# Performance work log

Hardware: AMD Instinct MI355X
Metric: run time of the kernel (lower is better)

The kernel has to match this reference:

```python
import jax, jax.numpy as jnp
import numpy as np
from jax import lax

DN = ('NCDHW', 'OIDHW', 'NCDHW')
BN_EPS = 1e-5  # eval-mode BatchNorm3d with running_mean=0, running_var=1


def conv3d(x, w, b):
    y = lax.conv_general_dilated(x, w, window_strides=(1, 1, 1),
                                 padding=[(1, 1)] * 3, dimension_numbers=DN)
    return y + b[None, :, None, None, None]


def maxpool2(x):
    return lax.reduce_window(x, -jnp.inf, lax.max,
                             (1, 1, 2, 2, 2), (1, 1, 2, 2, 2), 'VALID')


def spline_block(x, cw, cb, knots, sw, w1, w2, g, beta):
    # SplineConv3d: conv -> (BSpline3D blend with SiLU) -> BN(eval) -> maxpool
    y = conv3d(x, cw, cb)                                   # [b,c,d,h,w]
    basis = jnp.maximum(y[..., None] - knots, 0.0) ** 3     # [b,c,d,h,w,k]
    sp = jnp.einsum('bcdhwk,ck->bcdhw', basis, sw)
    out = (w1[None, :, None, None, None] * sp
           + w2[None, :, None, None, None] * (y * jax.nn.sigmoid(y)))
    scale = (g / jnp.sqrt(1.0 + BN_EPS))[None, :, None, None, None]
    return maxpool2(out * scale + beta[None, :, None, None, None])


def setup_inputs() -> dict:
    key = jax.random.key(0)
    ks = iter(jax.random.split(key, 40))
    def nrm(shape, s=1.0):
        return jax.random.normal(next(ks), shape, dtype=jnp.float32) * s
    d = {}
    d['x'] = nrm((2, 1, 64, 64, 64))
    for cin, cout, t in [(1, 32, '1'), (32, 64, '2'), (64, 128, '3')]:
        d[f'c{t}_w'] = nrm((cout, cin, 3, 3, 3), 0.1)
        d[f'c{t}_b'] = nrm((cout,), 0.01)
        d[f'c{t}_knots'] = jnp.linspace(-1.0, 1.0, 10).astype(jnp.float32)
        d[f'c{t}_sw'] = nrm((cout, 10), 0.2)
        d[f'c{t}_w1'] = nrm((cout,), 0.2)
        d[f'c{t}_w2'] = nrm((cout,), 0.2)
        d[f'bn{t}_g'] = 1.0 + nrm((cout,), 0.1)
        d[f'bn{t}_b'] = nrm((cout,), 0.1)
    d['fc1_w'] = nrm((256, 128), 0.05)
    d['fc1_b'] = nrm((256,), 0.01)
    d['fc2_w'] = nrm((2, 256), 0.05)
    d['fc2_b'] = nrm((2,), 0.01)
    return d


def reference(x,
              c1_w, c1_b, c1_knots, c1_sw, c1_w1, c1_w2, bn1_g, bn1_b,
              c2_w, c2_b, c2_knots, c2_sw, c2_w1, c2_w2, bn2_g, bn2_b,
              c3_w, c3_b, c3_knots, c3_sw, c3_w1, c3_w2, bn3_g, bn3_b,
              fc1_w, fc1_b, fc2_w, fc2_b):
    h = spline_block(x, c1_w, c1_b, c1_knots, c1_sw, c1_w1, c1_w2, bn1_g, bn1_b)
    h = spline_block(h, c2_w, c2_b, c2_knots, c2_sw, c2_w1, c2_w2, bn2_g, bn2_b)
    h = spline_block(h, c3_w, c3_b, c3_knots, c3_sw, c3_w1, c3_w2, bn3_g, bn3_b)
    h = h.mean(axis=(2, 3, 4))          # AdaptiveAvgPool3d((1,1,1)) + flatten
    h = jax.nn.relu(h @ fc1_w.T + fc1_b)  # dropout is identity in eval mode
    return h @ fc2_w.T + fc2_b
```

## Files before the change

kernel.cpp:

```cpp
#include <hip/hip_runtime.h>
#include <math.h>


#define GLOBAL_AS __attribute__((address_space(1)))
#define LDS_AS    __attribute__((address_space(3)))

static __device__ __forceinline__ void async_ld16(const float* g, float* l) {
    __builtin_amdgcn_global_load_lds((const GLOBAL_AS void*)g, (LDS_AS void*)l,
                                     16, 0, 0);
}

__global__ __launch_bounds__(256) void repack_kernel(
    const float* __restrict__ w1, const float* __restrict__ w2,
    const float* __restrict__ w3,
    float* __restrict__ o1, float* __restrict__ o2, float* __restrict__ o3)
{
    const int i = blockIdx.x * 256 + threadIdx.x;
    const float* src;
    float* dst;
    if (i < 32)            { src = w1 + i * 27;           dst = o1 + i * 28; }
    else if (i < 2080)     { const int j = i - 32;   src = w2 + j * 27; dst = o2 + j * 28; }
    else if (i < 10272)    { const int j = i - 2080; src = w3 + j * 27; dst = o3 + j * 28; }
    else return;
#pragma unroll
    for (int t = 0; t < 27; t++) dst[t] = src[t];
    dst[27] = 0.0f;
}

template <int TPB_, int CIN, int CSPLIT, int G,
          int WDT, int WHT, int WWT, int BD, int BH, int BW>
__global__ __launch_bounds__(TPB_, 2) void spline_block_kernel(
    const float* __restrict__ x,
    const float4* __restrict__ wpk,
    const float* __restrict__ cb,
    const float* __restrict__ knots,
    const float* __restrict__ sw,
    const float* __restrict__ w1,
    const float* __restrict__ w2,
    const float* __restrict__ g,
    const float* __restrict__ beta,
    const float* __restrict__ zbuf,
    float* __restrict__ out,
    int N, int Cout, int D, int H, int W,
    int ntiles, int nthw, int ntw)
{
    constexpr int NSW    = BD * BH * BW;
    constexpr int NW     = TPB_ / 64;
    constexpr int CPG    = CIN / CSPLIT;
    constexpr int ID     = 2 * WDT + 2;
    constexpr int IH     = 2 * WHT + 2;
    constexpr int CHK    = (WWT + 4) / 2;
    constexpr int PITCH  = CHK * 4;
    constexpr int ROWS   = ID * IH;
    constexpr int CHUNKS = ROWS * CHK;
    constexpr int PHYS   = CHUNKS * 4;
    constexpr int NCH    = (CHUNKS + 63) / 64;
    constexpr int BUFS   = (CPG > 1) ? 2 : 1;
    static_assert(NW == NSW * CSPLIT, "waves = spatial-tiles x cin-split");
    static_assert(WDT * WHT * WWT == 64, "one wave per spatial tile");
    static_assert(CIN % CSPLIT == 0, "cin divisible");
    static_assert(G == 4, "weight half-loop assumes G==4");
    static_assert(NCH <= 32, "mask fits u32");
    static_assert(NCH == 6, "s_waitcnt vmcnt(6) literal assumes 6 issues/cin");
    static_assert(CSPLIT == 1 ||
                  (CSPLIT - 1) * 64 * G * 8 <= NW * BUFS * PHYS,
                  "reduction scratch fits in tile");

    __shared__ __align__(16) float tile[NW][BUFS][PHYS];
    __shared__ float4 stbl[G * 11];

    const int PD = D >> 1, PH = H >> 1, PW = W >> 1;
    const int groups = Cout / G;
    const int tid  = threadIdx.x;
    const int wv   = tid >> 6;
    const int lane = tid & 63;
    const int sw_  = wv % NSW;
    const int cg   = wv / NSW;

    const int bx      = blockIdx.x;
    const int tile_id = bx % ntiles;
    const int t1      = bx / ntiles;
    const int grp     = t1 % groups;
    const int n       = t1 / groups;
    const int c0      = grp * G;
    const int cinbase = cg * CPG;
    const int cinbase_u = __builtin_amdgcn_readfirstlane(cinbase);

    const int td  = tile_id / nthw;
    const int rem = tile_id % nthw;
    const int th_ = rem / ntw;
    const int tw_ = rem % ntw;

    for (int i = tid; i < G * 11; i += TPB_) {
        const int gg  = i / 11;
        const int cnt = i % 11;
        const int c   = c0 + gg;
        float A = 0.f, B3 = 0.f, C3 = 0.f, Dd = 0.f;
        for (int j = 0; j < cnt; j++) {
            const float s = sw[c * 10 + j];
            const float k = knots[j];
            A  += s;
            B3 += 3.0f * s * k;
            C3 += 3.0f * s * k * k;
            Dd += s * k * k * k;
        }
        stbl[i] = make_float4(A, B3, C3, Dd);
    }

    const int swd = sw_ / (BH * BW);
    const int r2  = sw_ % (BH * BW);
    const int swh = r2 / BW;
    const int sww = r2 % BW;
    const int pd0 = td  * (BD * WDT) + swd * WDT;
    const int ph0 = th_ * (BH * WHT) + swh * WHT;
    const int pw0 = tw_ * (BW * WWT) + sww * WWT;

    const int pwl = lane % WWT;
    const int phl = (lane / WWT) % WHT;
    const int pdl = lane / (WWT * WHT);

    const int d0 = 2 * pd0 - 1, h0 = 2 * ph0 - 1;
    const int w0 = 2 * pw0 - 1;
    const int wb = w0 & ~3;
    const int woff = w0 - wb;

    int off[NCH];
    unsigned vm = 0;
#pragma unroll
    for (int k = 0; k < NCH; k++) {
        const int chunk = lane + 64 * k;
        const int row = chunk / CHK, cs = chunk - row * CHK;
        const int dz = row / IH, hy = row - dz * IH;
        const int dd = d0 + dz, hh = h0 + hy;
        const int wsd = wb + cs * 4;
        const bool ok = (chunk < CHUNKS) &
                        ((unsigned)dd < (unsigned)D) &
                        ((unsigned)hh < (unsigned)H) &
                        ((unsigned)wsd < (unsigned)W);
        off[k] = ok ? (dd * H + hh) * W + wsd : 0;
        vm |= (unsigned)ok << k;
    }

    const size_t chstride = (size_t)D * H * W;
    const float* xn = x + (size_t)n * CIN * chstride;

    float acc[G][8];
#pragma unroll
    for (int gg = 0; gg < G; gg++)
#pragma unroll
        for (int i = 0; i < 8; i++) acc[gg][i] = 0.0f;

    __syncthreads();

    auto stage = [&](int ci, int buf) {
        const float* xc = xn + (size_t)ci * chstride;
        float* dst = &tile[wv][buf][0];
#pragma unroll
        for (int k = 0; k < NCH; k++) {
            const int chunk = lane + 64 * k;
            if ((k + 1) * 64 <= CHUNKS || chunk < CHUNKS) {
                const float* src = ((vm >> k) & 1) ? (xc + off[k]) : zbuf;
                async_ld16(src, dst + chunk * 4);
            }
        }
    };

    stage(cinbase_u, 0);

#pragma unroll 1
    for (int s = 0; s < CPG; s++) {
        const int cur = s & (BUFS - 1);
        if (s + 1 < CPG) {
            stage(cinbase_u + s + 1, cur ^ 1);
            asm volatile("s_waitcnt vmcnt(6)" ::: "memory");
        } else {
            asm volatile("s_waitcnt vmcnt(0)" ::: "memory");
        }

        const int ci_u = cinbase_u + s;
        const float4* wq = wpk + (size_t)(c0 * CIN + ci_u) * 7;

        const float* tb = &tile[wv][cur][0];
        float r[64];
#pragma unroll
        for (int dz = 0; dz < 4; dz++)
#pragma unroll
        for (int dy = 0; dy < 4; dy++) {
            const int rb = ((2 * pdl + dz) * IH + (2 * phl + dy)) * PITCH +
                           woff + 2 * pwl;
            r[(dz * 4 + dy) * 4 + 0] = tb[rb + 0];
            r[(dz * 4 + dy) * 4 + 1] = tb[rb + 1];
            r[(dz * 4 + dy) * 4 + 2] = tb[rb + 2];
            r[(dz * 4 + dy) * 4 + 3] = tb[rb + 3];
        }

#pragma unroll
        for (int half = 0; half < 2; half++) {
            float4 q[2][7];
#pragma unroll
            for (int gh = 0; gh < 2; gh++)
#pragma unroll
                for (int ch = 0; ch < 7; ch++)
                    q[gh][ch] = wq[(size_t)(half * 2 + gh) * (CIN * 7) + ch];
#pragma unroll
            for (int gh = 0; gh < 2; gh++) {
                const int gg = half * 2 + gh;
#pragma unroll
                for (int ch = 0; ch < 7; ch++) {
#pragma unroll
                    for (int j = 0; j < 4; j++) {
                        const int tap = ch * 4 + j;
                        if (tap < 27) {
                            const float wvj = (j == 0) ? q[gh][ch].x
                                            : (j == 1) ? q[gh][ch].y
                                            : (j == 2) ? q[gh][ch].z
                                            : q[gh][ch].w;
                            const int kd = tap / 9, kh = (tap % 9) / 3, kw = tap % 3;
#pragma unroll
                            for (int od = 0; od < 2; od++)
#pragma unroll
                            for (int oh = 0; oh < 2; oh++)
#pragma unroll
                            for (int ow = 0; ow < 2; ow++)
                                acc[gg][(od * 2 + oh) * 2 + ow] =
                                    fmaf(wvj,
                                         r[((od + kd) * 4 + (oh + kh)) * 4 + (ow + kw)],
                                         acc[gg][(od * 2 + oh) * 2 + ow]);
                        }
                    }
                }
            }
        }
    }

    float* af = &acc[0][0];
    if (CSPLIT > 1) {
        __syncthreads();
        float* scratch = &tile[0][0][0];
        if (cg > 0) {
#pragma unroll
            for (int idx = 0; idx < G * 8; idx++)
                scratch[(idx * (CSPLIT - 1) + (cg - 1)) * 64 + lane] = af[idx];
        }
        __syncthreads();
        if (cg == 0) {
#pragma unroll
            for (int idx = 0; idx < G * 8; idx++) {
                float s2 = af[idx];
                for (int j = 0; j < CSPLIT - 1; j++)
                    s2 += scratch[(idx * (CSPLIT - 1) + j) * 64 + lane];
                af[idx] = s2;
            }
        }
    }

    if (cg == 0) {
        const int pdg = pd0 + pdl, phg = ph0 + phl, pwg = pw0 + pwl;
#pragma unroll
        for (int gg = 0; gg < G; gg++) {
            const int c = c0 + gg;
            const float bias = cb[c];
            const float W1 = w1[c], W2 = w2[c];
            const float scale = g[c] * rsqrtf(1.0f + 1e-5f);
            const float bb = beta[c];

            float m = -INFINITY;
#pragma unroll
            for (int i = 0; i < 8; i++) {
                const float y = acc[gg][i] + bias;
                int idx = (int)floorf((y + 1.0f) * 4.5f) + 1;
                idx = min(max(idx, 0), 10);
                const float4 cf = stbl[gg * 11 + idx];
                const float sp = ((cf.x * y - cf.y) * y + cf.z) * y - cf.w;
                const float silu = y / (1.0f + __expf(-y));
                const float o = fmaf(W1 * sp + W2 * silu, scale, bb);
                m = fmaxf(m, o);
            }
            out[((size_t)(n * Cout + c) * PD + pdg) * PH * PW + phg * PW + pwg] = m;
        }
    }
}

__global__ __launch_bounds__(256) void head_kernel(
    const float* __restrict__ h,
    const float* __restrict__ fw1, const float* __restrict__ fb1,
    const float* __restrict__ fw2, const float* __restrict__ fb2,
    float* __restrict__ out)
{
    __shared__ float pooled[256];
    __shared__ float hbuf[2][256];
    const int tid = threadIdx.x, w = tid >> 6, lane = tid & 63;
    for (int p = w; p < 256; p += 4) {
        const float* row = h + (size_t)p * 512;
        float s = 0.0f;
#pragma unroll
        for (int i = 0; i < 8; i++) s += row[lane + 64 * i];
#pragma unroll
        for (int o = 32; o > 0; o >>= 1) s += __shfl_down(s, o, 64);
        if (lane == 0) pooled[p] = s * (1.0f / 512.0f);
    }
    __syncthreads();
    const int j = tid;
#pragma unroll
    for (int nn = 0; nn < 2; nn++) {
        float s = fb1[j];
        for (int k = 0; k < 128; k++)
            s = fmaf(pooled[nn * 128 + k], fw1[j * 128 + k], s);
        hbuf[nn][j] = fmaxf(s, 0.0f);
    }
    __syncthreads();
    const int wid = j >> 6, l2 = j & 63;
    const int nn = wid >> 1, oo = wid & 1;
    float s = 0.0f;
    for (int k = l2; k < 256; k += 64) s += hbuf[nn][k] * fw2[oo * 256 + k];
#pragma unroll
    for (int o = 32; o > 0; o >>= 1) s += __shfl_down(s, o, 64);
    if (l2 == 0) out[nn * 2 + oo] = s + fb2[oo];
}

extern "C" void kernel_launch(void* const* d_in, const int* in_sizes, int n_in,
                              void* d_out, int out_size, void* d_ws, size_t ws_size,
                              hipStream_t stream) {
    const float* x      = (const float*)d_in[0];
    const float* c1_w   = (const float*)d_in[1];
    const float* c1_b   = (const float*)d_in[2];
    const float* c1_kn  = (const float*)d_in[3];
    const float* c1_sw  = (const float*)d_in[4];
    const float* c1_w1  = (const float*)d_in[5];
    const float* c1_w2  = (const float*)d_in[6];
    const float* bn1_g  = (const float*)d_in[7];
    const float* bn1_b  = (const float*)d_in[8];
    const float* c2_w   = (const float*)d_in[9];
    const float* c2_b   = (const float*)d_in[10];
    const float* c2_kn  = (const float*)d_in[11];
    const float* c2_sw  = (const float*)d_in[12];
    const float* c2_w1  = (const float*)d_in[13];
    const float* c2_w2  = (const float*)d_in[14];
    const float* bn2_g  = (const float*)d_in[15];
    const float* bn2_b  = (const float*)d_in[16];
    const float* c3_w   = (const float*)d_in[17];
    const float* c3_b   = (const float*)d_in[18];
    const float* c3_kn  = (const float*)d_in[19];
    const float* c3_sw  = (const float*)d_in[20];
    const float* c3_w1  = (const float*)d_in[21];
    const float* c3_w2  = (const float*)d_in[22];
    const float* bn3_g  = (const float*)d_in[23];
    const float* bn3_b  = (const float*)d_in[24];
    const float* fc1_w  = (const float*)d_in[25];
    const float* fc1_b  = (const float*)d_in[26];
    const float* fc2_w  = (const float*)d_in[27];
    const float* fc2_b  = (const float*)d_in[28];

    float* ws = (float*)d_ws;
    float* h1     = ws;
    float* h2     = h1 + 2097152;
    float* h3     = h2 + 524288;
    float* pooled = h3 + 131072;
    float* zbuf   = pooled + 256;
    float* wp1    = zbuf + 16;
    float* wp2    = wp1 + 896;
    float* wp3    = wp2 + 57344;

    hipMemsetAsync(zbuf, 0, 64, stream);

    repack_kernel<<<dim3(41), dim3(256), 0, stream>>>(c1_w, c2_w, c3_w,
                                                      wp1, wp2, wp3);

    spline_block_kernel<128, 1, 1, 4, 2, 4, 8, 1, 1, 2>
        <<<dim3(4096), dim3(128), 0, stream>>>(
        x, (const float4*)wp1, c1_b, c1_kn, c1_sw, c1_w1, c1_w2, bn1_g, bn1_b,
        zbuf, h1, 2, 32, 64, 64, 64, 256, 16, 2);
    spline_block_kernel<128, 32, 2, 4, 2, 4, 8, 1, 1, 1>
        <<<dim3(2048), dim3(128), 0, stream>>>(
        h1, (const float4*)wp2, c2_b, c2_kn, c2_sw, c2_w1, c2_w2, bn2_g, bn2_b,
        zbuf, h2, 2, 64, 32, 32, 32, 64, 8, 2);
    spline_block_kernel<256, 64, 4, 4, 2, 4, 8, 1, 1, 1>
        <<<dim3(512), dim3(256), 0, stream>>>(
        h2, (const float4*)wp3, c3_b, c3_kn, c3_sw, c3_w1, c3_w2, bn3_g, bn3_b,
        zbuf, h3, 2, 128, 16, 16, 16, 8, 2, 1);
    head_kernel<<<dim3(1), dim3(256), 0, stream>>>(h3, fc1_w, fc1_b, fc2_w, fc2_b,
                                                   (float*)d_out);
}
```

Before: 369.5 us.

## Use zero-padded activation buffers to drop bounds masking and misaligned staging

```diff
diff --git a/kernel.cpp b/kernel.cpp
--- a/kernel.cpp
+++ b/kernel.cpp
@@ -10,21 +10,38 @@
                                      16, 0, 0);
 }
 
-__global__ __launch_bounds__(256) void repack_kernel(
+__global__ __launch_bounds__(256) void prep_kernel(
+    const float* __restrict__ x,
     const float* __restrict__ w1, const float* __restrict__ w2,
     const float* __restrict__ w3,
+    float* __restrict__ xp,
     float* __restrict__ o1, float* __restrict__ o2, float* __restrict__ o3)
 {
-    const int i = blockIdx.x * 256 + threadIdx.x;
-    const float* src;
-    float* dst;
-    if (i < 32)            { src = w1 + i * 27;           dst = o1 + i * 28; }
-    else if (i < 2080)     { const int j = i - 32;   src = w2 + j * 27; dst = o2 + j * 28; }
-    else if (i < 10272)    { const int j = i - 2080; src = w3 + j * 27; dst = o3 + j * 28; }
-    else return;
-#pragma unroll
-    for (int t = 0; t < 27; t++) dst[t] = src[t];
-    dst[27] = 0.0f;
+    const int b = blockIdx.x;
+    if (b < 41) {
+        const int i = b * 256 + threadIdx.x;
+        const float* src;
+        float* dst;
+        if (i < 32)         { src = w1 + i * 27;              dst = o1 + i * 28; }
+        else if (i < 2080)  { const int j = i - 32;    src = w2 + j * 27; dst = o2 + j * 28; }
+        else if (i < 10272) { const int j = i - 2080;  src = w3 + j * 27; dst = o3 + j * 28; }
+        else return;
+#pragma unroll
+        for (int t = 0; t < 27; t++) dst[t] = src[t];
+        dst[27] = 0.0f;
+    } else {
+        const int idx = (b - 41) * 256 + threadIdx.x;
+        if (idx >= 2 * 66 * 66 * 68) return;
+        const int wp = idx % 68;
+        int t = idx / 68;
+        const int hp = t % 66; t /= 66;
+        const int dp = t % 66;
+        const int nn = t / 66;
+        float v = 0.0f;
+        if (dp >= 1 && dp <= 64 && hp >= 1 && hp <= 64 && wp >= 1 && wp <= 64)
+            v = x[(((size_t)nn * 64 + dp - 1) * 64 + hp - 1) * 64 + wp - 1];
+        xp[idx] = v;
+    }
 }
 
 template <int TPB_, int CIN, int CSPLIT, int G,
@@ -39,9 +56,10 @@
     const float* __restrict__ w2,
     const float* __restrict__ g,
     const float* __restrict__ beta,
-    const float* __restrict__ zbuf,
     float* __restrict__ out,
-    int N, int Cout, int D, int H, int W,
+    int N, int Cout,
+    int ICH, int IHP, int IWP,
+    int ODP, int OHP, int OWP, int OPAD,
     int ntiles, int nthw, int ntw)
 {
     constexpr int NSW    = BD * BH * BW;
@@ -49,27 +67,27 @@
     constexpr int CPG    = CIN / CSPLIT;
     constexpr int ID     = 2 * WDT + 2;
     constexpr int IH     = 2 * WHT + 2;
-    constexpr int CHK    = (WWT + 4) / 2;
+    constexpr int CHK    = 5;
     constexpr int PITCH  = CHK * 4;
     constexpr int ROWS   = ID * IH;
     constexpr int CHUNKS = ROWS * CHK;
-    constexpr int PHYS   = CHUNKS * 4;
+    constexpr int PHYS   = ROWS * PITCH;
     constexpr int NCH    = (CHUNKS + 63) / 64;
+    constexpr int TAIL   = CHUNKS & 63;
     constexpr int BUFS   = (CPG > 1) ? 2 : 1;
     static_assert(NW == NSW * CSPLIT, "waves = spatial-tiles x cin-split");
     static_assert(WDT * WHT * WWT == 64, "one wave per spatial tile");
+    static_assert(WDT == 2 && WHT == 4 && WWT == 8, "tile geometry fixed");
     static_assert(CIN % CSPLIT == 0, "cin divisible");
-    static_assert(G == 4, "weight half-loop assumes G==4");
-    static_assert(NCH <= 32, "mask fits u32");
-    static_assert(NCH == 6, "s_waitcnt vmcnt(6) literal assumes 6 issues/cin");
+    static_assert(G == 4, "acc layout assumes G==4");
+    static_assert(NCH == 5, "s_waitcnt vmcnt(5) literal assumes 5 issues/cin");
     static_assert(CSPLIT == 1 ||
-                  (CSPLIT - 1) * 64 * G * 8 <= NW * BUFS * PHYS,
+                  (CSPLIT - 1) * NSW * 64 * G * 8 <= NW * BUFS * PHYS,
                   "reduction scratch fits in tile");
 
     __shared__ __align__(16) float tile[NW][BUFS][PHYS];
     __shared__ float4 stbl[G * 11];
 
-    const int PD = D >> 1, PH = H >> 1, PW = W >> 1;
     const int groups = Cout / G;
     const int tid  = threadIdx.x;
     const int wv   = tid >> 6;
@@ -84,7 +102,6 @@
     const int n       = t1 / groups;
     const int c0      = grp * G;
     const int cinbase = cg * CPG;
-    const int cinbase_u = __builtin_amdgcn_readfirstlane(cinbase);
 
     const int td  = tile_id / nthw;
     const int rem = tile_id % nthw;
@@ -119,30 +136,15 @@
     const int phl = (lane / WWT) % WHT;
     const int pdl = lane / (WWT * WHT);
 
-    const int d0 = 2 * pd0 - 1, h0 = 2 * ph0 - 1;
-    const int w0 = 2 * pw0 - 1;
-    const int wb = w0 & ~3;
-    const int woff = w0 - wb;
-
     int off[NCH];
-    unsigned vm = 0;
 #pragma unroll
     for (int k = 0; k < NCH; k++) {
         const int chunk = lane + 64 * k;
         const int row = chunk / CHK, cs = chunk - row * CHK;
         const int dz = row / IH, hy = row - dz * IH;
-        const int dd = d0 + dz, hh = h0 + hy;
-        const int wsd = wb + cs * 4;
-        const bool ok = (chunk < CHUNKS) &
-                        ((unsigned)dd < (unsigned)D) &
-                        ((unsigned)hh < (unsigned)H) &
-                        ((unsigned)wsd < (unsigned)W);
-        off[k] = ok ? (dd * H + hh) * W + wsd : 0;
-        vm |= (unsigned)ok << k;
-    }
-
-    const size_t chstride = (size_t)D * H * W;
-    const float* xn = x + (size_t)n * CIN * chstride;
+        off[k] = ((2 * pd0 + dz) * IHP + (2 * ph0 + hy)) * IWP +
+                 2 * pw0 + cs * 4;
+    }
 
     float acc[G][8];
 #pragma unroll
@@ -153,33 +155,29 @@
     __syncthreads();
 
     auto stage = [&](int ci, int buf) {
-        const float* xc = xn + (size_t)ci * chstride;
+        const float* xc = x + ((size_t)n * CIN + ci) * ICH;
         float* dst = &tile[wv][buf][0];
 #pragma unroll
         for (int k = 0; k < NCH; k++) {
             const int chunk = lane + 64 * k;
-            if ((k + 1) * 64 <= CHUNKS || chunk < CHUNKS) {
-                const float* src = ((vm >> k) & 1) ? (xc + off[k]) : zbuf;
-                async_ld16(src, dst + chunk * 4);
-            }
+            if ((k + 1) * 64 <= CHUNKS || lane < TAIL)
+                async_ld16(xc + off[k], dst + chunk * 4);
         }
     };
 
-    stage(cinbase_u, 0);
+    stage(cinbase, 0);
 
 #pragma unroll 1
     for (int s = 0; s < CPG; s++) {
         const int cur = s & (BUFS - 1);
         if (s + 1 < CPG) {
-            stage(cinbase_u + s + 1, cur ^ 1);
-            asm volatile("s_waitcnt vmcnt(6)" ::: "memory");
+            stage(cinbase + s + 1, cur ^ 1);
+            asm volatile("s_waitcnt vmcnt(5)" ::: "memory");
         } else {
             asm volatile("s_waitcnt vmcnt(0)" ::: "memory");
         }
 
-        const int ci_u = cinbase_u + s;
-        const float4* wq = wpk + (size_t)(c0 * CIN + ci_u) * 7;
-
+        const int ci = cinbase + s;
         const float* tb = &tile[wv][cur][0];
         float r[64];
 #pragma unroll
@@ -187,46 +185,39 @@
 #pragma unroll
         for (int dy = 0; dy < 4; dy++) {
             const int rb = ((2 * pdl + dz) * IH + (2 * phl + dy)) * PITCH +
-                           woff + 2 * pwl;
-            r[(dz * 4 + dy) * 4 + 0] = tb[rb + 0];
-            r[(dz * 4 + dy) * 4 + 1] = tb[rb + 1];
-            r[(dz * 4 + dy) * 4 + 2] = tb[rb + 2];
-            r[(dz * 4 + dy) * 4 + 3] = tb[rb + 3];
-        }
-
-#pragma unroll
-        for (int half = 0; half < 2; half++) {
-            float4 q[2][7];
-#pragma unroll
-            for (int gh = 0; gh < 2; gh++)
-#pragma unroll
-                for (int ch = 0; ch < 7; ch++)
-                    q[gh][ch] = wq[(size_t)(half * 2 + gh) * (CIN * 7) + ch];
-#pragma unroll
-            for (int gh = 0; gh < 2; gh++) {
-                const int gg = half * 2 + gh;
-#pragma unroll
-                for (int ch = 0; ch < 7; ch++) {
-#pragma unroll
-                    for (int j = 0; j < 4; j++) {
-                        const int tap = ch * 4 + j;
-                        if (tap < 27) {
-                            const float wvj = (j == 0) ? q[gh][ch].x
-                                            : (j == 1) ? q[gh][ch].y
-                                            : (j == 2) ? q[gh][ch].z
-                                            : q[gh][ch].w;
-                            const int kd = tap / 9, kh = (tap % 9) / 3, kw = tap % 3;
-#pragma unroll
-                            for (int od = 0; od < 2; od++)
-#pragma unroll
-                            for (int oh = 0; oh < 2; oh++)
-#pragma unroll
-                            for (int ow = 0; ow < 2; ow++)
-                                acc[gg][(od * 2 + oh) * 2 + ow] =
-                                    fmaf(wvj,
-                                         r[((od + kd) * 4 + (oh + kh)) * 4 + (ow + kw)],
-                                         acc[gg][(od * 2 + oh) * 2 + ow]);
-                        }
+                           2 * pwl;
+            const float2 a = *reinterpret_cast<const float2*>(&tb[rb]);
+            const float2 b = *reinterpret_cast<const float2*>(&tb[rb + 2]);
+            const int base = (dz * 4 + dy) * 4;
+            r[base + 0] = a.x; r[base + 1] = a.y;
+            r[base + 2] = b.x; r[base + 3] = b.y;
+        }
+
+#pragma unroll
+        for (int gg = 0; gg < G; gg++) {
+            const float4* wp = wpk + ((size_t)(c0 + gg) * CIN + ci) * 7;
+            float4 q[7];
+#pragma unroll
+            for (int ch = 0; ch < 7; ch++) q[ch] = wp[ch];
+#pragma unroll
+            for (int ch = 0; ch < 7; ch++) {
+#pragma unroll
+                for (int j = 0; j < 4; j++) {
+                    const int tap = ch * 4 + j;
+                    if (tap < 27) {
+                        const float wvj = (j == 0) ? q[ch].x : (j == 1) ? q[ch].y
+                                        : (j == 2) ? q[ch].z : q[ch].w;
+                        const int kd = tap / 9, kh = (tap % 9) / 3, kw = tap % 3;
+#pragma unroll
+                        for (int od = 0; od < 2; od++)
+#pragma unroll
+                        for (int oh = 0; oh < 2; oh++)
+#pragma unroll
+                        for (int ow = 0; ow < 2; ow++)
+                            acc[gg][(od * 2 + oh) * 2 + ow] =
+                                fmaf(wvj,
+                                     r[((od + kd) * 4 + (oh + kh)) * 4 + (ow + kw)],
+                                     acc[gg][(od * 2 + oh) * 2 + ow]);
                     }
                 }
             }
@@ -240,7 +231,8 @@
         if (cg > 0) {
 #pragma unroll
             for (int idx = 0; idx < G * 8; idx++)
-                scratch[(idx * (CSPLIT - 1) + (cg - 1)) * 64 + lane] = af[idx];
+                scratch[((idx * (CSPLIT - 1) + (cg - 1)) * NSW + sw_) * 64 + lane]
+                    = af[idx];
         }
         __syncthreads();
         if (cg == 0) {
@@ -248,7 +240,7 @@
             for (int idx = 0; idx < G * 8; idx++) {
                 float s2 = af[idx];
                 for (int j = 0; j < CSPLIT - 1; j++)
-                    s2 += scratch[(idx * (CSPLIT - 1) + j) * 64 + lane];
+                    s2 += scratch[((idx * (CSPLIT - 1) + j) * NSW + sw_) * 64 + lane];
                 af[idx] = s2;
             }
         }
@@ -276,7 +268,8 @@
                 const float o = fmaf(W1 * sp + W2 * silu, scale, bb);
                 m = fmaxf(m, o);
             }
-            out[((size_t)(n * Cout + c) * PD + pdg) * PH * PW + phg * PW + pwg] = m;
+            out[(((size_t)(n * Cout + c) * ODP + pdg + OPAD) * OHP +
+                 phg + OPAD) * OWP + pwg + OPAD] = m;
         }
     }
 }
@@ -352,32 +345,32 @@
     const float* fc2_b  = (const float*)d_in[28];
 
     float* ws = (float*)d_ws;
-    float* h1     = ws;
-    float* h2     = h1 + 2097152;
-    float* h3     = h2 + 524288;
-    float* pooled = h3 + 131072;
-    float* zbuf   = pooled + 256;
-    float* wp1    = zbuf + 16;
+    float* x_pad  = ws;
+    float* h1_pad = x_pad + 592416;
+    float* h2_pad = h1_pad + 2663424;
+    float* h3     = h2_pad + 829440;
+    float* wp1    = h3 + 131072;
     float* wp2    = wp1 + 896;
     float* wp3    = wp2 + 57344;
 
-    hipMemsetAsync(zbuf, 0, 64, stream);
-
-    repack_kernel<<<dim3(41), dim3(256), 0, stream>>>(c1_w, c2_w, c3_w,
-                                                      wp1, wp2, wp3);
-
-    spline_block_kernel<128, 1, 1, 4, 2, 4, 8, 1, 1, 2>
-        <<<dim3(4096), dim3(128), 0, stream>>>(
-        x, (const float4*)wp1, c1_b, c1_kn, c1_sw, c1_w1, c1_w2, bn1_g, bn1_b,
-        zbuf, h1, 2, 32, 64, 64, 64, 256, 16, 2);
-    spline_block_kernel<128, 32, 2, 4, 2, 4, 8, 1, 1, 1>
-        <<<dim3(2048), dim3(128), 0, stream>>>(
-        h1, (const float4*)wp2, c2_b, c2_kn, c2_sw, c2_w1, c2_w2, bn2_g, bn2_b,
-        zbuf, h2, 2, 64, 32, 32, 32, 64, 8, 2);
+    hipMemsetAsync(h1_pad, 0, 2663424 * sizeof(float), stream);
+    hipMemsetAsync(h2_pad, 0, 829440 * sizeof(float), stream);
+
+    prep_kernel<<<dim3(41 + 2315), dim3(256), 0, stream>>>(
+        x, c1_w, c2_w, c3_w, x_pad, wp1, wp2, wp3);
+
+    spline_block_kernel<256, 1, 1, 4, 2, 4, 8, 1, 1, 4>
+        <<<dim3(2048), dim3(256), 0, stream>>>(
+        x_pad, (const float4*)wp1, c1_b, c1_kn, c1_sw, c1_w1, c1_w2, bn1_g, bn1_b,
+        h1_pad, 2, 32, 296208, 66, 68, 34, 34, 36, 1, 128, 8, 1);
+    spline_block_kernel<256, 32, 2, 4, 2, 4, 8, 1, 1, 2>
+        <<<dim3(1024), dim3(256), 0, stream>>>(
+        h1_pad, (const float4*)wp2, c2_b, c2_kn, c2_sw, c2_w1, c2_w2, bn2_g, bn2_b,
+        h2_pad, 2, 64, 41616, 34, 36, 18, 18, 20, 1, 32, 4, 1);
     spline_block_kernel<256, 64, 4, 4, 2, 4, 8, 1, 1, 1>
         <<<dim3(512), dim3(256), 0, stream>>>(
-        h2, (const float4*)wp3, c3_b, c3_kn, c3_sw, c3_w1, c3_w2, bn3_g, bn3_b,
-        zbuf, h3, 2, 128, 16, 16, 16, 8, 2, 1);
+        h2_pad, (const float4*)wp3, c3_b, c3_kn, c3_sw, c3_w1, c3_w2, bn3_g, bn3_b,
+        h3, 2, 128, 6480, 18, 20, 8, 8, 8, 0, 8, 2, 1);
     head_kernel<<<dim3(1), dim3(256), 0, stream>>>(h3, fc1_w, fc1_b, fc2_w, fc2_b,
                                                    (float*)d_out);
 }
```

Measured after the change: 378.1 us. 1.02x slower.

## Loop over output-channel groups per staged tile in layer 1; widen blocks

Applied to the files above, without the earlier changes.

```diff
diff --git a/kernel.cpp b/kernel.cpp
--- a/kernel.cpp
+++ b/kernel.cpp
@@ -27,7 +27,7 @@
     dst[27] = 0.0f;
 }
 
-template <int TPB_, int CIN, int CSPLIT, int G,
+template <int TPB_, int CIN, int CSPLIT, int G, int CGO,
           int WDT, int WHT, int WWT, int BD, int BH, int BW>
 __global__ __launch_bounds__(TPB_, 2) void spline_block_kernel(
     const float* __restrict__ x,
@@ -44,6 +44,7 @@
     int N, int Cout, int D, int H, int W,
     int ntiles, int nthw, int ntw)
 {
+    constexpr int GTOT   = G * CGO;
     constexpr int NSW    = BD * BH * BW;
     constexpr int NW     = TPB_ / 64;
     constexpr int CPG    = CIN / CSPLIT;
@@ -59,18 +60,20 @@
     static_assert(NW == NSW * CSPLIT, "waves = spatial-tiles x cin-split");
     static_assert(WDT * WHT * WWT == 64, "one wave per spatial tile");
     static_assert(CIN % CSPLIT == 0, "cin divisible");
-    static_assert(G == 4, "weight half-loop assumes G==4");
+    static_assert(G == 4, "acc layout assumes G==4");
+    static_assert(CGO == 1 || (CSPLIT == 1 && CIN == 1),
+                  "multi-cout-group only for the CIN=1 single-step layer");
     static_assert(NCH <= 32, "mask fits u32");
     static_assert(NCH == 6, "s_waitcnt vmcnt(6) literal assumes 6 issues/cin");
     static_assert(CSPLIT == 1 ||
-                  (CSPLIT - 1) * 64 * G * 8 <= NW * BUFS * PHYS,
+                  (CSPLIT - 1) * NSW * 64 * G * 8 <= NW * BUFS * PHYS,
                   "reduction scratch fits in tile");
 
     __shared__ __align__(16) float tile[NW][BUFS][PHYS];
-    __shared__ float4 stbl[G * 11];
+    __shared__ float4 stbl[GTOT * 11];
 
     const int PD = D >> 1, PH = H >> 1, PW = W >> 1;
-    const int groups = Cout / G;
+    const int groups = Cout / GTOT;
     const int tid  = threadIdx.x;
     const int wv   = tid >> 6;
     const int lane = tid & 63;
@@ -82,7 +85,7 @@
     const int t1      = bx / ntiles;
     const int grp     = t1 % groups;
     const int n       = t1 / groups;
-    const int c0      = grp * G;
+    const int c0      = grp * GTOT;
     const int cinbase = cg * CPG;
     const int cinbase_u = __builtin_amdgcn_readfirstlane(cinbase);
 
@@ -91,7 +94,7 @@
     const int th_ = rem / ntw;
     const int tw_ = rem % ntw;
 
-    for (int i = tid; i < G * 11; i += TPB_) {
+    for (int i = tid; i < GTOT * 11; i += TPB_) {
         const int gg  = i / 11;
         const int cnt = i % 11;
         const int c   = c0 + gg;
@@ -165,21 +168,44 @@
         }
     };
 
-    stage(cinbase_u, 0);
+    const int pdg = pd0 + pdl, phg = ph0 + phl, pwg = pw0 + pwl;
+    auto epilogue = [&](int gbase) {
+#pragma unroll
+        for (int gg = 0; gg < G; gg++) {
+            const int c = c0 + gbase + gg;
+            const float bias = cb[c];
+            const float W1 = w1[c], W2 = w2[c];
+            const float scale = g[c] * rsqrtf(1.0f + 1e-5f);
+            const float bb = beta[c];
+            float m = -INFINITY;
+#pragma unroll
+            for (int i = 0; i < 8; i++) {
+                const float y = acc[gg][i] + bias;
+                int idx = (int)floorf((y + 1.0f) * 4.5f) + 1;
+                idx = min(max(idx, 0), 10);
+                const float4 cf = stbl[(gbase + gg) * 11 + idx];
+                const float sp = ((cf.x * y - cf.y) * y + cf.z) * y - cf.w;
+                const float silu = y / (1.0f + __expf(-y));
+                const float o = fmaf(W1 * sp + W2 * silu, scale, bb);
+                m = fmaxf(m, o);
+            }
+            out[((size_t)(n * Cout + c) * PD + pdg) * PH * PW + phg * PW + pwg] = m;
+        }
+    };
+
+    stage(cinbase, 0);
 
 #pragma unroll 1
     for (int s = 0; s < CPG; s++) {
         const int cur = s & (BUFS - 1);
         if (s + 1 < CPG) {
-            stage(cinbase_u + s + 1, cur ^ 1);
+            stage(cinbase + s + 1, cur ^ 1);
             asm volatile("s_waitcnt vmcnt(6)" ::: "memory");
         } else {
             asm volatile("s_waitcnt vmcnt(0)" ::: "memory");
         }
 
         const int ci_u = cinbase_u + s;
-        const float4* wq = wpk + (size_t)(c0 * CIN + ci_u) * 7;
-
         const float* tb = &tile[wv][cur][0];
         float r[64];
 #pragma unroll
@@ -194,28 +220,33 @@
             r[(dz * 4 + dy) * 4 + 3] = tb[rb + 3];
         }
 
-#pragma unroll
-        for (int half = 0; half < 2; half++) {
-            float4 q[2][7];
-#pragma unroll
-            for (int gh = 0; gh < 2; gh++)
-#pragma unroll
-                for (int ch = 0; ch < 7; ch++)
-                    q[gh][ch] = wq[(size_t)(half * 2 + gh) * (CIN * 7) + ch];
-#pragma unroll
-            for (int gh = 0; gh < 2; gh++) {
-                const int gg = half * 2 + gh;
+#pragma unroll 1
+        for (int cgo = 0; cgo < CGO; cgo++) {
+            if constexpr (CGO > 1) {
+#pragma unroll
+                for (int gg = 0; gg < G; gg++)
+#pragma unroll
+                    for (int i = 0; i < 8; i++) acc[gg][i] = 0.0f;
+            }
+            const int cbase = cgo * G;
+#pragma unroll
+            for (int gg = 0; gg < G; gg++) {
+                const float4* wq = wpk +
+                    ((size_t)(c0 + cbase + gg) * CIN + ci_u) * 7;
+                float4 q[7];
+#pragma unroll
+                for (int ch = 0; ch < 7; ch++) q[ch] = wq[ch];
 #pragma unroll
                 for (int ch = 0; ch < 7; ch++) {
 #pragma unroll
                     for (int j = 0; j < 4; j++) {
                         const int tap = ch * 4 + j;
                         if (tap < 27) {
-                            const float wvj = (j == 0) ? q[gh][ch].x
-                                            : (j == 1) ? q[gh][ch].y
-                                            : (j == 2) ? q[gh][ch].z
-                                            : q[gh][ch].w;
-                            const int kd = tap / 9, kh = (tap % 9) / 3, kw = tap % 3;
+                            const float wvj = (j == 0) ? q[ch].x
+                                            : (j == 1) ? q[ch].y
+                                            : (j == 2) ? q[ch].z : q[ch].w;
+                            const int kd = tap / 9, kh = (tap % 9) / 3,
+                                      kw = tap % 3;
 #pragma unroll
                             for (int od = 0; od < 2; od++)
 #pragma unroll
@@ -230,54 +261,33 @@
                     }
                 }
             }
-        }
-    }
-
-    float* af = &acc[0][0];
-    if (CSPLIT > 1) {
-        __syncthreads();
-        float* scratch = &tile[0][0][0];
-        if (cg > 0) {
-#pragma unroll
-            for (int idx = 0; idx < G * 8; idx++)
-                scratch[(idx * (CSPLIT - 1) + (cg - 1)) * 64 + lane] = af[idx];
-        }
-        __syncthreads();
-        if (cg == 0) {
-#pragma unroll
-            for (int idx = 0; idx < G * 8; idx++) {
-                float s2 = af[idx];
-                for (int j = 0; j < CSPLIT - 1; j++)
-                    s2 += scratch[(idx * (CSPLIT - 1) + j) * 64 + lane];
-                af[idx] = s2;
-            }
-        }
-    }
-
-    if (cg == 0) {
-        const int pdg = pd0 + pdl, phg = ph0 + phl, pwg = pw0 + pwl;
-#pragma unroll
-        for (int gg = 0; gg < G; gg++) {
-            const int c = c0 + gg;
-            const float bias = cb[c];
-            const float W1 = w1[c], W2 = w2[c];
-            const float scale = g[c] * rsqrtf(1.0f + 1e-5f);
-            const float bb = beta[c];
-
-            float m = -INFINITY;
-#pragma unroll
-            for (int i = 0; i < 8; i++) {
-                const float y = acc[gg][i] + bias;
-                int idx = (int)floorf((y + 1.0f) * 4.5f) + 1;
-                idx = min(max(idx, 0), 10);
-                const float4 cf = stbl[gg * 11 + idx];
-                const float sp = ((cf.x * y - cf.y) * y + cf.z) * y - cf.w;
-                const float silu = y / (1.0f + __expf(-y));
-                const float o = fmaf(W1 * sp + W2 * silu, scale, bb);
-                m = fmaxf(m, o);
-            }
-            out[((size_t)(n * Cout + c) * PD + pdg) * PH * PW + phg * PW + pwg] = m;
-        }
+            if constexpr (CGO > 1) epilogue(cbase);
+        }
+    }
+
+    if constexpr (CGO == 1) {
+        float* af = &acc[0][0];
+        if (CSPLIT > 1) {
+            __syncthreads();
+            float* scratch = &tile[0][0][0];
+            if (cg > 0) {
+#pragma unroll
+                for (int idx = 0; idx < G * 8; idx++)
+                    scratch[((idx * (CSPLIT - 1) + (cg - 1)) * NSW + sw_) * 64 + lane]
+                        = af[idx];
+            }
+            __syncthreads();
+            if (cg == 0) {
+#pragma unroll
+                for (int idx = 0; idx < G * 8; idx++) {
+                    float s2 = af[idx];
+                    for (int j = 0; j < CSPLIT - 1; j++)
+                        s2 += scratch[((idx * (CSPLIT - 1) + j) * NSW + sw_) * 64 + lane];
+                    af[idx] = s2;
+                }
+            }
+        }
+        if (cg == 0) epilogue(0);
     }
 }
 
@@ -366,15 +376,15 @@
     repack_kernel<<<dim3(41), dim3(256), 0, stream>>>(c1_w, c2_w, c3_w,
                                                       wp1, wp2, wp3);
 
-    spline_block_kernel<128, 1, 1, 4, 2, 4, 8, 1, 1, 2>
-        <<<dim3(4096), dim3(128), 0, stream>>>(
+    spline_block_kernel<256, 1, 1, 4, 8, 2, 4, 8, 2, 2, 1>
+        <<<dim3(256), dim3(256), 0, stream>>>(
         x, (const float4*)wp1, c1_b, c1_kn, c1_sw, c1_w1, c1_w2, bn1_g, bn1_b,
-        zbuf, h1, 2, 32, 64, 64, 64, 256, 16, 2);
-    spline_block_kernel<128, 32, 2, 4, 2, 4, 8, 1, 1, 1>
-        <<<dim3(2048), dim3(128), 0, stream>>>(
+        zbuf, h1, 2, 32, 64, 64, 64, 128, 16, 4);
+    spline_block_kernel<256, 32, 2, 4, 1, 2, 4, 8, 1, 1, 2>
+        <<<dim3(1024), dim3(256), 0, stream>>>(
         h1, (const float4*)wp2, c2_b, c2_kn, c2_sw, c2_w1, c2_w2, bn2_g, bn2_b,
-        zbuf, h2, 2, 64, 32, 32, 32, 64, 8, 2);
-    spline_block_kernel<256, 64, 4, 4, 2, 4, 8, 1, 1, 1>
+        zbuf, h2, 2, 64, 32, 32, 32, 32, 4, 1);
+    spline_block_kernel<256, 64, 4, 4, 1, 2, 4, 8, 1, 1, 1>
         <<<dim3(512), dim3(256), 0, stream>>>(
         h2, (const float4*)wp3, c3_b, c3_kn, c3_sw, c3_w1, c3_w2, bn3_g, bn3_b,
         zbuf, h3, 2, 128, 16, 16, 16, 8, 2, 1);
```

New measurement: 377.4 us. 1.02x slower.
